# Optimization experiments

Measured on AMD Instinct MI355X. Metric: run time of the kernel, lower is better.

The kernel has to match this reference:

```python
import jax, jax.numpy as jnp
import numpy as np

# dims: S temporal frames, B batch, N queries/batch, K knn neighbors, M img samples, C channels
S, B, N, K, M, C = 3, 2, 2048, 16, 32, 256
W_SCALE = 0.02


def setup_inputs() -> dict:
    key = jax.random.key(0)
    ks = jax.random.split(key, 24)
    f = lambda k, shp: jax.random.normal(k, shp, dtype=jnp.float32)
    w = lambda k, shp: f(k, shp) * W_SCALE
    mask = jax.random.uniform(ks[5], (B, N, M)) > 0.3
    mask = mask.at[..., 0].set(True)  # every query attends to >=1 sample (mirrors `valid` filter)
    return {
        "pts_query_feats": f(ks[0], (B, N, C)),
        "pts_query_pe": f(ks[1], (B, N, C)),
        "knn_feat": f(ks[2], (S, B, N, K, C)),
        "knn_pe": f(ks[3], (S, B, N, K, C)),
        "sampled_feat": f(ks[4], (B, N, M, C)),
        # per-seq temporal MHA (1 head) weights, stacked over S
        "Wq_t": w(ks[6], (S, C, C)), "Wk_t": w(ks[7], (S, C, C)),
        "Wv_t": w(ks[8], (S, C, C)), "Wo_t": w(ks[9], (S, C, C)),
        "bq_t": jnp.zeros((S, C)), "bk_t": jnp.zeros((S, C)),
        "bv_t": jnp.zeros((S, C)), "bo_t": jnp.zeros((S, C)),
        # cross-sensor MHA (1 head) weights
        "Wq_c": w(ks[10], (C, C)), "Wk_c": w(ks[11], (C, C)),
        "Wv_c": w(ks[12], (C, C)), "Wo_c": w(ks[13], (C, C)),
        "bq_c": jnp.zeros((C,)), "bk_c": jnp.zeros((C,)),
        "bv_c": jnp.zeros((C,)), "bo_c": jnp.zeros((C,)),
        "mask": mask,
    }


def reference(pts_query_feats, pts_query_pe, knn_feat, knn_pe, sampled_feat,
              Wq_t, Wk_t, Wv_t, Wo_t, bq_t, bk_t, bv_t, bo_t,
              Wq_c, Wk_c, Wv_c, Wo_c, bq_c, bk_c, bv_c, bo_c, mask):
    C_ = pts_query_feats.shape[-1]
    scale = 1.0 / np.float32(np.sqrt(C_))

    # query = pts features + positional embedding (with_pos_embed)
    q0 = pts_query_feats + pts_query_pe                     # [B,N,C]
    kv = knn_feat + knn_pe                                  # [S,B,N,K,C]

    # per-seq temporal attention (seq_len cloned 1-head MHA), summed over seq
    q = jnp.einsum('bnc,scd->sbnd', q0, Wq_t) + bq_t[:, None, None, :]
    k = jnp.einsum('sbnkc,scd->sbnkd', kv, Wk_t) + bk_t[:, None, None, None, :]
    v = jnp.einsum('sbnkc,scd->sbnkd', kv, Wv_t) + bv_t[:, None, None, None, :]
    attn = jax.nn.softmax(jnp.einsum('sbnd,sbnkd->sbnk', q, k) * scale, axis=-1)
    av = jnp.einsum('sbnk,sbnkd->sbnd', attn, v)
    out = (jnp.einsum('sbnd,sde->sbne', av, Wo_t) + bo_t[:, None, None, :]).sum(0)  # [B,N,C]

    # cross-sensor attention: query = temporal output, key/value = sampled image feats,
    # boolean mask (True = valid; original passes attn_mask = ~mask)
    q2 = out @ Wq_c + bq_c                                  # [B,N,C]
    k2 = jnp.einsum('bnmc,cd->bnmd', sampled_feat, Wk_c) + bk_c
    v2 = jnp.einsum('bnmc,cd->bnmd', sampled_feat, Wv_c) + bv_c
    s2 = jnp.einsum('bnd,bnmd->bnm', q2, k2) * scale
    s2 = jnp.where(mask, s2, jnp.float32(-1e30))
    a2 = jax.nn.softmax(s2, axis=-1)
    cs = jnp.einsum('bnm,bnmd->bnd', a2, v2) @ Wo_c + bo_c  # [B,N,C]
    return cs
```

## Files before the change

### kernel.cpp

```cpp
#include <hip/hip_runtime.h>
#include <hip/hip_bf16.h>
#include <math.h>

#define SS 3
#define BB 2
#define NN 2048
#define KK 16
#define MM 32
#define CC 256
#define BN_TOT 4096
#define SCALE 0.0625f

#define OFF_ACAT   0
#define OFF_ABCAT  196608
#define OFF_VOCAT  197376
#define OFF_VBSUM  393984
#define OFF_AC     394240
#define OFF_ABC    459776
#define OFF_VOC    460032
#define OFF_VBC    525568
#define OFF_A2     525824
#define OFF_AB2    722432
#define OFF_QKCAT  722688
#define OFF_WKV    3868416
#define OFF_QK2    7014144
#define OFF_WS2    8062720

__device__ __forceinline__ void combine_body(const float* __restrict__ L,
                                             const float* __restrict__ R,
                                             float* __restrict__ O, int ldo,
                                             int nt, int r0) {
    __shared__ float L8[8][256];
    int t = threadIdx.x;
#pragma unroll
    for (int j = 0; j < 8; ++j) L8[j][t] = L[(r0 + j) * 256 + t];
    __syncthreads();
    float acc[8] = {};
    if (nt) {
        const float* rp = R + t * 256;
        for (int d = 0; d < 256; d += 4) {
            float4 rv = *(const float4*)(rp + d);
#pragma unroll
            for (int j = 0; j < 8; ++j) {
                float4 lv = *(const float4*)(&L8[j][d]);
                acc[j] += lv.x * rv.x + lv.y * rv.y + lv.z * rv.z + lv.w * rv.w;
            }
        }
    } else {
        for (int d = 0; d < 256; d += 4) {
            float r0v = R[(d + 0) * 256 + t];
            float r1v = R[(d + 1) * 256 + t];
            float r2v = R[(d + 2) * 256 + t];
            float r3v = R[(d + 3) * 256 + t];
#pragma unroll
            for (int j = 0; j < 8; ++j) {
                float4 lv = *(const float4*)(&L8[j][d]);
                acc[j] += lv.x * r0v + lv.y * r1v + lv.z * r2v + lv.w * r3v;
            }
        }
    }
#pragma unroll
    for (int j = 0; j < 8; ++j) O[(r0 + j) * ldo + t] = acc[j];
}

__global__ __launch_bounds__(256) void combine1(
    const float* __restrict__ Wq_t, const float* __restrict__ Wk_t,
    const float* __restrict__ Wv_t, const float* __restrict__ Wo_t,
    const float* __restrict__ Wq_c, const float* __restrict__ Wk_c,
    const float* __restrict__ Wv_c, const float* __restrict__ Wo_c,
    float* __restrict__ ws) {
    int job = blockIdx.x >> 5, rb = blockIdx.x & 31;
    const float *L, *R; float* O; int ldo, nt;
    if (job < 3)       { L = Wq_t + job * 65536; R = Wk_t + job * 65536; O = ws + OFF_ACAT + job * 256;    ldo = 768; nt = 1; }
    else if (job < 6)  { int s = job - 3; L = Wv_t + s * 65536; R = Wo_t + s * 65536; O = ws + OFF_VOCAT + s * 65536; ldo = 256; nt = 0; }
    else if (job == 6) { L = Wq_c; R = Wk_c; O = ws + OFF_AC;  ldo = 256; nt = 1; }
    else               { L = Wv_c; R = Wo_c; O = ws + OFF_VOC; ldo = 256; nt = 0; }
    combine_body(L, R, O, ldo, nt, rb * 8);
}

__global__ __launch_bounds__(256) void bias1(
    const float* __restrict__ Wk_t, const float* __restrict__ Wo_t,
    const float* __restrict__ bq_t, const float* __restrict__ bv_t, const float* __restrict__ bo_t,
    const float* __restrict__ Wk_c, const float* __restrict__ Wo_c,
    const float* __restrict__ bq_c, const float* __restrict__ bv_c, const float* __restrict__ bo_c,
    float* __restrict__ ws) {
    int t = threadIdx.x;
    for (int s = 0; s < 3; ++s) {
        const float* wk = Wk_t + (s * 256 + t) * 256;
        const float* bq = bq_t + s * 256;
        float a = 0;
        for (int d = 0; d < 256; ++d) a += bq[d] * wk[d];
        ws[OFF_ABCAT + s * 256 + t] = a;
    }
    float v = 0;
    for (int s = 0; s < 3; ++s) {
        const float* wo = Wo_t + s * 65536;
        const float* bv = bv_t + s * 256;
        float a = 0;
        for (int d = 0; d < 256; ++d) a += bv[d] * wo[d * 256 + t];
        v += a + bo_t[s * 256 + t];
    }
    ws[OFF_VBSUM + t] = v;
    { float a = 0; const float* wk = Wk_c + t * 256;
      for (int d = 0; d < 256; ++d) a += bq_c[d] * wk[d];
      ws[OFF_ABC + t] = a; }
    { float a = 0;
      for (int d = 0; d < 256; ++d) a += bv_c[d] * Wo_c[d * 256 + t];
      ws[OFF_VBC + t] = a + bo_c[t]; }
}

__global__ __launch_bounds__(256) void combine2(float* __restrict__ ws) {
    int wg = blockIdx.x;
    if (wg < 96) {
        combine_body(ws + OFF_VOCAT, ws + OFF_AC, ws + OFF_A2, 256, 0, wg * 8);
    } else {
        int t = threadIdx.x;
        float a = 0;
        const float* vb = ws + OFF_VBSUM;
        const float* Ac = ws + OFF_AC;
        for (int e = 0; e < 256; ++e) a += vb[e] * Ac[e * 256 + t];
        ws[OFF_AB2 + t] = a + ws[OFF_ABC + t];
    }
}

__global__ __launch_bounds__(256) void gemm_bias(
    const float* __restrict__ A, const float* __restrict__ Aadd, int lda,
    const float* __restrict__ Bm, int ldb,
    const float* __restrict__ bias,
    float* __restrict__ out, int ldo, int Kd) {
    __shared__ float As[16][64];
    __shared__ float Bs[16][68];
    int tid = threadIdx.x;
    int bm = blockIdx.x * 64, bn = blockIdx.y * 64;
    int tx = tid & 15, ty = tid >> 4;
    float acc[4][4] = {};
    int ar = tid >> 2, ak = (tid & 3) * 4;
    int bk = tid >> 4, bq = (tid & 15) * 4;
    const float* Ab  = A + (size_t)(bm + ar) * lda + ak;
    const float* A2b = Aadd ? Aadd + (size_t)(bm + ar) * lda + ak : nullptr;
    const float* Bb  = Bm + (size_t)bk * ldb + bn + bq;
    for (int k0 = 0; k0 < Kd; k0 += 16) {
        float4 av = *(const float4*)(Ab + k0);
        if (Aadd) {
            float4 a2 = *(const float4*)(A2b + k0);
            av.x += a2.x; av.y += a2.y; av.z += a2.z; av.w += a2.w;
        }
        As[ak + 0][ar] = av.x; As[ak + 1][ar] = av.y;
        As[ak + 2][ar] = av.z; As[ak + 3][ar] = av.w;
        *(float4*)(&Bs[bk][bq]) = *(const float4*)(Bb + (size_t)k0 * ldb);
        __syncthreads();
#pragma unroll
        for (int kk = 0; kk < 16; ++kk) {
            float4 a4 = *(const float4*)(&As[kk][ty * 4]);
            float4 b4 = *(const float4*)(&Bs[kk][tx * 4]);
            float aa[4] = {a4.x, a4.y, a4.z, a4.w};
            float bb[4] = {b4.x, b4.y, b4.z, b4.w};
#pragma unroll
            for (int i = 0; i < 4; ++i)
#pragma unroll
                for (int j = 0; j < 4; ++j) acc[i][j] += aa[i] * bb[j];
        }
        __syncthreads();
    }
#pragma unroll
    for (int i = 0; i < 4; ++i) {
        int row = bm + ty * 4 + i;
        float b0 = bias[bn + tx * 4 + 0], b1 = bias[bn + tx * 4 + 1];
        float b2 = bias[bn + tx * 4 + 2], b3 = bias[bn + tx * 4 + 3];
        float4 o;
        o.x = acc[i][0] + b0; o.y = acc[i][1] + b1;
        o.z = acc[i][2] + b2; o.w = acc[i][3] + b3;
        *(float4*)(&out[(size_t)row * ldo + bn + tx * 4]) = o;
    }
}

__global__ __launch_bounds__(256) void attn_temporal(
    const float* __restrict__ knn_feat, const float* __restrict__ knn_pe,
    const float* __restrict__ qk_cat, float* __restrict__ wkv_cat) {
    int wg = blockIdx.x;
    int s = wg >> 12, bn = wg & 4095;
    int t = threadIdx.x;
    int lane = t & 63, wv = t >> 6;
    size_t base = (size_t)wg * 4096 + t;
    float kv[16];
#pragma unroll
    for (int k = 0; k < 16; ++k)
        kv[k] = knn_feat[base + k * 256] + knn_pe[base + k * 256];
    float qv = qk_cat[(size_t)bn * 768 + s * 256 + t];
    __shared__ float red[4][16];
    __shared__ float sc[16];
#pragma unroll
    for (int k = 0; k < 16; ++k) {
        float v = qv * kv[k];
#pragma unroll
        for (int off = 32; off; off >>= 1) v += __shfl_xor(v, off, 64);
        if (lane == 0) red[wv][k] = v;
    }
    __syncthreads();
    if (t < 16) sc[t] = (red[0][t] + red[1][t] + red[2][t] + red[3][t]) * SCALE;
    __syncthreads();
    float mx = -1e30f;
#pragma unroll
    for (int k = 0; k < 16; ++k) mx = fmaxf(mx, sc[k]);
    float p[16], den = 0.f;
#pragma unroll
    for (int k = 0; k < 16; ++k) { p[k] = __expf(sc[k] - mx); den += p[k]; }
    float o = 0.f;
#pragma unroll
    for (int k = 0; k < 16; ++k) o += p[k] * kv[k];
    wkv_cat[(size_t)bn * 768 + s * 256 + t] = o * (1.f / den);
}

__global__ __launch_bounds__(256) void attn_cross(
    const float* __restrict__ sampled, const int* __restrict__ mask,
    const float* __restrict__ qk2, float* __restrict__ ws2) {
    int bn = blockIdx.x;
    int t = threadIdx.x;
    int lane = t & 63, wv = t >> 6;
    size_t base = (size_t)bn * 8192 + t;
    float smp[32];
#pragma unroll
    for (int m = 0; m < 32; ++m) smp[m] = sampled[base + m * 256];
    float qv = qk2[(size_t)bn * 256 + t];
    __shared__ float red[4][32];
    __shared__ float sc[32];
#pragma unroll
    for (int m = 0; m < 32; ++m) {
        float v = qv * smp[m];
#pragma unroll
        for (int off = 32; off; off >>= 1) v += __shfl_xor(v, off, 64);
        if (lane == 0) red[wv][m] = v;
    }
    __syncthreads();
    if (t < 32) {
        float v = (red[0][t] + red[1][t] + red[2][t] + red[3][t]) * SCALE;
        sc[t] = mask[(size_t)bn * 32 + t] ? v : -1e30f;
    }
    __syncthreads();
    float mx = -1e30f;
#pragma unroll
    for (int m = 0; m < 32; ++m) mx = fmaxf(mx, sc[m]);
    float den = 0.f, o = 0.f;
#pragma unroll
    for (int m = 0; m < 32; ++m) {
        float p = __expf(sc[m] - mx);
        den += p; o += p * smp[m];
    }
    ws2[(size_t)bn * 256 + t] = o / den;
}

extern "C" void kernel_launch(void* const* d_in, const int* in_sizes, int n_in,
                              void* d_out, int out_size, void* d_ws, size_t ws_size,
                              hipStream_t stream) {
    const float* feats    = (const float*)d_in[0];
    const float* pe       = (const float*)d_in[1];
    const float* knn_feat = (const float*)d_in[2];
    const float* knn_pe   = (const float*)d_in[3];
    const float* sampled  = (const float*)d_in[4];
    const float* Wq_t = (const float*)d_in[5];
    const float* Wk_t = (const float*)d_in[6];
    const float* Wv_t = (const float*)d_in[7];
    const float* Wo_t = (const float*)d_in[8];
    const float* bq_t = (const float*)d_in[9];
    const float* bv_t = (const float*)d_in[11];
    const float* bo_t = (const float*)d_in[12];
    const float* Wq_c = (const float*)d_in[13];
    const float* Wk_c = (const float*)d_in[14];
    const float* Wv_c = (const float*)d_in[15];
    const float* Wo_c = (const float*)d_in[16];
    const float* bq_c = (const float*)d_in[17];
    const float* bv_c = (const float*)d_in[19];
    const float* bo_c = (const float*)d_in[20];
    const int*   mask = (const int*)d_in[21];
    float* ws  = (float*)d_ws;
    float* out = (float*)d_out;

    hipLaunchKernelGGL(combine1, dim3(256), dim3(256), 0, stream,
                       Wq_t, Wk_t, Wv_t, Wo_t, Wq_c, Wk_c, Wv_c, Wo_c, ws);
    hipLaunchKernelGGL(bias1, dim3(1), dim3(256), 0, stream,
                       Wk_t, Wo_t, bq_t, bv_t, bo_t, Wk_c, Wo_c, bq_c, bv_c, bo_c, ws);
    hipLaunchKernelGGL(combine2, dim3(97), dim3(256), 0, stream, ws);
    hipLaunchKernelGGL(gemm_bias, dim3(64, 12), dim3(256), 0, stream,
                       feats, pe, 256, ws + OFF_ACAT, 768, ws + OFF_ABCAT,
                       ws + OFF_QKCAT, 768, 256);
    hipLaunchKernelGGL(attn_temporal, dim3(12288), dim3(256), 0, stream,
                       knn_feat, knn_pe, ws + OFF_QKCAT, ws + OFF_WKV);
    hipLaunchKernelGGL(gemm_bias, dim3(64, 4), dim3(256), 0, stream,
                       ws + OFF_WKV, nullptr, 768, ws + OFF_A2, 256, ws + OFF_AB2,
                       ws + OFF_QK2, 256, 768);
    hipLaunchKernelGGL(attn_cross, dim3(4096), dim3(256), 0, stream,
                       sampled, mask, ws + OFF_QK2, ws + OFF_WS2);
    hipLaunchKernelGGL(gemm_bias, dim3(64, 4), dim3(256), 0, stream,
                       ws + OFF_WS2, nullptr, 256, ws + OFF_VOC, 256, ws + OFF_VBC,
                       out, 256, 256);
}
```

Baseline: 730.1 us.

## Wave-per-unit attention kernels, fold bias kernel into combine, drop GEMM B staging

The temporal attention kernel now gives each 64-lane wavefront one (s,b,n) unit, using float4 loads and a transpose-style shuffle reduction. This removes the LDS reductions and __syncthreads barriers that the old one-block-per-unit layout needed. The cross attention kernel splits the 32 samples across 4 waves with float4 loads and combines partial outputs through LDS. The single-block bias kernel is merged into combine1 as 5 extra blocks, saving a launch and its serial tail. gemm_bias now reads B directly from global memory instead of staging it in LDS, which may raise global traffic in exchange for fewer LDS stores.

```diff
diff --git a/kernel.cpp b/kernel.cpp
--- a/kernel.cpp
+++ b/kernel.cpp
@@ -68,7 +68,40 @@
     const float* __restrict__ Wv_t, const float* __restrict__ Wo_t,
     const float* __restrict__ Wq_c, const float* __restrict__ Wk_c,
     const float* __restrict__ Wv_c, const float* __restrict__ Wo_c,
+    const float* __restrict__ bq_t, const float* __restrict__ bv_t,
+    const float* __restrict__ bo_t,
+    const float* __restrict__ bq_c, const float* __restrict__ bv_c,
+    const float* __restrict__ bo_c,
     float* __restrict__ ws) {
+    int t = threadIdx.x;
+    if (blockIdx.x >= 256) {
+        int jb = blockIdx.x - 256;
+        if (jb < 3) {
+            const float* wk = Wk_t + (jb * 256 + t) * 256;
+            const float* bq = bq_t + jb * 256;
+            float a = 0;
+            for (int d = 0; d < 256; ++d) a += bq[d] * wk[d];
+            ws[OFF_ABCAT + jb * 256 + t] = a;
+        } else if (jb == 3) {
+            float v = 0;
+            for (int s = 0; s < 3; ++s) {
+                const float* wo = Wo_t + s * 65536;
+                const float* bv = bv_t + s * 256;
+                float a = 0;
+                for (int d = 0; d < 256; ++d) a += bv[d] * wo[d * 256 + t];
+                v += a + bo_t[s * 256 + t];
+            }
+            ws[OFF_VBSUM + t] = v;
+        } else {
+            float a = 0; const float* wk = Wk_c + t * 256;
+            for (int d = 0; d < 256; ++d) a += bq_c[d] * wk[d];
+            ws[OFF_ABC + t] = a;
+            float b = 0;
+            for (int d = 0; d < 256; ++d) b += bv_c[d] * Wo_c[d * 256 + t];
+            ws[OFF_VBC + t] = b + bo_c[t];
+        }
+        return;
+    }
     int job = blockIdx.x >> 5, rb = blockIdx.x & 31;
     const float *L, *R; float* O; int ldo, nt;
     if (job < 3)       { L = Wq_t + job * 65536; R = Wk_t + job * 65536; O = ws + OFF_ACAT + job * 256;    ldo = 768; nt = 1; }
@@ -76,37 +109,6 @@
     else if (job == 6) { L = Wq_c; R = Wk_c; O = ws + OFF_AC;  ldo = 256; nt = 1; }
     else               { L = Wv_c; R = Wo_c; O = ws + OFF_VOC; ldo = 256; nt = 0; }
     combine_body(L, R, O, ldo, nt, rb * 8);
-}
-
-__global__ __launch_bounds__(256) void bias1(
-    const float* __restrict__ Wk_t, const float* __restrict__ Wo_t,
-    const float* __restrict__ bq_t, const float* __restrict__ bv_t, const float* __restrict__ bo_t,
-    const float* __restrict__ Wk_c, const float* __restrict__ Wo_c,
-    const float* __restrict__ bq_c, const float* __restrict__ bv_c, const float* __restrict__ bo_c,
-    float* __restrict__ ws) {
-    int t = threadIdx.x;
-    for (int s = 0; s < 3; ++s) {
-        const float* wk = Wk_t + (s * 256 + t) * 256;
-        const float* bq = bq_t + s * 256;
-        float a = 0;
-        for (int d = 0; d < 256; ++d) a += bq[d] * wk[d];
-        ws[OFF_ABCAT + s * 256 + t] = a;
-    }
-    float v = 0;
-    for (int s = 0; s < 3; ++s) {
-        const float* wo = Wo_t + s * 65536;
-        const float* bv = bv_t + s * 256;
-        float a = 0;
-        for (int d = 0; d < 256; ++d) a += bv[d] * wo[d * 256 + t];
-        v += a + bo_t[s * 256 + t];
-    }
-    ws[OFF_VBSUM + t] = v;
-    { float a = 0; const float* wk = Wk_c + t * 256;
-      for (int d = 0; d < 256; ++d) a += bq_c[d] * wk[d];
-      ws[OFF_ABC + t] = a; }
-    { float a = 0;
-      for (int d = 0; d < 256; ++d) a += bv_c[d] * Wo_c[d * 256 + t];
-      ws[OFF_VBC + t] = a + bo_c[t]; }
 }
 
 __global__ __launch_bounds__(256) void combine2(float* __restrict__ ws) {
@@ -128,17 +130,15 @@
     const float* __restrict__ Bm, int ldb,
     const float* __restrict__ bias,
     float* __restrict__ out, int ldo, int Kd) {
-    __shared__ float As[16][64];
-    __shared__ float Bs[16][68];
+    __shared__ float As[16][68];
     int tid = threadIdx.x;
     int bm = blockIdx.x * 64, bn = blockIdx.y * 64;
     int tx = tid & 15, ty = tid >> 4;
     float acc[4][4] = {};
     int ar = tid >> 2, ak = (tid & 3) * 4;
-    int bk = tid >> 4, bq = (tid & 15) * 4;
     const float* Ab  = A + (size_t)(bm + ar) * lda + ak;
     const float* A2b = Aadd ? Aadd + (size_t)(bm + ar) * lda + ak : nullptr;
-    const float* Bb  = Bm + (size_t)bk * ldb + bn + bq;
+    const float* Bb  = Bm + bn + tx * 4;
     for (int k0 = 0; k0 < Kd; k0 += 16) {
         float4 av = *(const float4*)(Ab + k0);
         if (Aadd) {
@@ -147,12 +147,11 @@
         }
         As[ak + 0][ar] = av.x; As[ak + 1][ar] = av.y;
         As[ak + 2][ar] = av.z; As[ak + 3][ar] = av.w;
-        *(float4*)(&Bs[bk][bq]) = *(const float4*)(Bb + (size_t)k0 * ldb);
         __syncthreads();
 #pragma unroll
         for (int kk = 0; kk < 16; ++kk) {
+            float4 b4 = *(const float4*)(Bb + (size_t)(k0 + kk) * ldb);
             float4 a4 = *(const float4*)(&As[kk][ty * 4]);
-            float4 b4 = *(const float4*)(&Bs[kk][tx * 4]);
             float aa[4] = {a4.x, a4.y, a4.z, a4.w};
             float bb[4] = {b4.x, b4.y, b4.z, b4.w};
 #pragma unroll
@@ -177,38 +176,68 @@
 __global__ __launch_bounds__(256) void attn_temporal(
     const float* __restrict__ knn_feat, const float* __restrict__ knn_pe,
     const float* __restrict__ qk_cat, float* __restrict__ wkv_cat) {
-    int wg = blockIdx.x;
-    int s = wg >> 12, bn = wg & 4095;
-    int t = threadIdx.x;
-    int lane = t & 63, wv = t >> 6;
-    size_t base = (size_t)wg * 4096 + t;
-    float kv[16];
+    int unit = blockIdx.x * 4 + (threadIdx.x >> 6);
+    int lane = threadIdx.x & 63;
+    int s = unit >> 12, bn = unit & 4095;
+    size_t base = (size_t)unit * 4096 + lane * 4;
+    float4 kv[16];
+#pragma unroll
+    for (int k = 0; k < 16; ++k) {
+        float4 f = *(const float4*)(knn_feat + base + k * 256);
+        float4 p = *(const float4*)(knn_pe   + base + k * 256);
+        kv[k] = make_float4(f.x + p.x, f.y + p.y, f.z + p.z, f.w + p.w);
+    }
+    float4 q = *(const float4*)(qk_cat + (size_t)bn * 768 + s * 256 + lane * 4);
+    float v[16];
 #pragma unroll
     for (int k = 0; k < 16; ++k)
-        kv[k] = knn_feat[base + k * 256] + knn_pe[base + k * 256];
-    float qv = qk_cat[(size_t)bn * 768 + s * 256 + t];
-    __shared__ float red[4][16];
-    __shared__ float sc[16];
+        v[k] = q.x * kv[k].x + q.y * kv[k].y + q.z * kv[k].z + q.w * kv[k].w;
+    { int hi = lane & 32;
+#pragma unroll
+      for (int j = 0; j < 8; ++j) {
+          float send = hi ? v[j] : v[j + 8];
+          float keep = hi ? v[j + 8] : v[j];
+          v[j] = keep + __shfl_xor(send, 32, 64);
+      } }
+    { int hi = lane & 16;
+#pragma unroll
+      for (int j = 0; j < 4; ++j) {
+          float send = hi ? v[j] : v[j + 4];
+          float keep = hi ? v[j + 4] : v[j];
+          v[j] = keep + __shfl_xor(send, 16, 64);
+      } }
+    { int hi = lane & 8;
+#pragma unroll
+      for (int j = 0; j < 2; ++j) {
+          float send = hi ? v[j] : v[j + 2];
+          float keep = hi ? v[j + 2] : v[j];
+          v[j] = keep + __shfl_xor(send, 8, 64);
+      } }
+    { int hi = lane & 4;
+      float send = hi ? v[0] : v[1];
+      float keep = hi ? v[1] : v[0];
+      v[0] = keep + __shfl_xor(send, 4, 64); }
+    float r = v[0];
+    r += __shfl_xor(r, 1, 64);
+    r += __shfl_xor(r, 2, 64);
+    float sc[16];
+#pragma unroll
+    for (int k = 0; k < 16; ++k) sc[k] = __shfl(r, k << 2, 64) * SCALE;
+    float mx = sc[0];
+#pragma unroll
+    for (int k = 1; k < 16; ++k) mx = fmaxf(mx, sc[k]);
+    float den = 0.f;
+#pragma unroll
+    for (int k = 0; k < 16; ++k) { sc[k] = __expf(sc[k] - mx); den += sc[k]; }
+    float inv = 1.f / den;
+    float ox = 0, oy = 0, oz = 0, ow = 0;
 #pragma unroll
     for (int k = 0; k < 16; ++k) {
-        float v = qv * kv[k];
-#pragma unroll
-        for (int off = 32; off; off >>= 1) v += __shfl_xor(v, off, 64);
-        if (lane == 0) red[wv][k] = v;
-    }
-    __syncthreads();
-    if (t < 16) sc[t] = (red[0][t] + red[1][t] + red[2][t] + red[3][t]) * SCALE;
-    __syncthreads();
-    float mx = -1e30f;
-#pragma unroll
-    for (int k = 0; k < 16; ++k) mx = fmaxf(mx, sc[k]);
-    float p[16], den = 0.f;
-#pragma unroll
-    for (int k = 0; k < 16; ++k) { p[k] = __expf(sc[k] - mx); den += p[k]; }
-    float o = 0.f;
-#pragma unroll
-    for (int k = 0; k < 16; ++k) o += p[k] * kv[k];
-    wkv_cat[(size_t)bn * 768 + s * 256 + t] = o * (1.f / den);
+        ox += sc[k] * kv[k].x; oy += sc[k] * kv[k].y;
+        oz += sc[k] * kv[k].z; ow += sc[k] * kv[k].w;
+    }
+    float4 o = make_float4(ox * inv, oy * inv, oz * inv, ow * inv);
+    *(float4*)(wkv_cat + (size_t)bn * 768 + s * 256 + lane * 4) = o;
 }
 
 __global__ __launch_bounds__(256) void attn_cross(
@@ -216,37 +245,76 @@
     const float* __restrict__ qk2, float* __restrict__ ws2) {
     int bn = blockIdx.x;
     int t = threadIdx.x;
-    int lane = t & 63, wv = t >> 6;
-    size_t base = (size_t)bn * 8192 + t;
-    float smp[32];
-#pragma unroll
-    for (int m = 0; m < 32; ++m) smp[m] = sampled[base + m * 256];
-    float qv = qk2[(size_t)bn * 256 + t];
-    __shared__ float red[4][32];
-    __shared__ float sc[32];
+    int w = t >> 6, lane = t & 63;
+    __shared__ float sc_lds[32];
+    __shared__ float obuf[4][256];
+    size_t base = (size_t)bn * 8192 + (size_t)(w * 8) * 256 + lane * 4;
+    float4 sm[8];
+#pragma unroll
+    for (int j = 0; j < 8; ++j) sm[j] = *(const float4*)(sampled + base + j * 256);
+    float4 q = *(const float4*)(qk2 + (size_t)bn * 256 + lane * 4);
+    float v[8];
+#pragma unroll
+    for (int j = 0; j < 8; ++j)
+        v[j] = q.x * sm[j].x + q.y * sm[j].y + q.z * sm[j].z + q.w * sm[j].w;
+    { int hi = lane & 32;
+#pragma unroll
+      for (int j = 0; j < 4; ++j) {
+          float send = hi ? v[j] : v[j + 4];
+          float keep = hi ? v[j + 4] : v[j];
+          v[j] = keep + __shfl_xor(send, 32, 64);
+      } }
+    { int hi = lane & 16;
+#pragma unroll
+      for (int j = 0; j < 2; ++j) {
+          float send = hi ? v[j] : v[j + 2];
+          float keep = hi ? v[j + 2] : v[j];
+          v[j] = keep + __shfl_xor(send, 16, 64);
+      } }
+    { int hi = lane & 8;
+      float send = hi ? v[0] : v[1];
+      float keep = hi ? v[1] : v[0];
+      v[0] = keep + __shfl_xor(send, 8, 64); }
+    float r = v[0];
+    r += __shfl_xor(r, 1, 64);
+    r += __shfl_xor(r, 2, 64);
+    r += __shfl_xor(r, 4, 64);
+    if ((lane & 7) == 0) {
+        int m = w * 8 + (lane >> 3);
+        int valid = mask[(size_t)bn * 32 + m];
+        sc_lds[m] = valid ? r * SCALE : -1e30f;
+    }
+    __syncthreads();
+    float scv[32];
+#pragma unroll
+    for (int i = 0; i < 8; ++i) {
+        float4 v4 = *(const float4*)(&sc_lds[i * 4]);
+        scv[i * 4 + 0] = v4.x; scv[i * 4 + 1] = v4.y;
+        scv[i * 4 + 2] = v4.z; scv[i * 4 + 3] = v4.w;
+    }
+    float mx = scv[0];
+#pragma unroll
+    for (int m = 1; m < 32; ++m) mx = fmaxf(mx, scv[m]);
+    float den = 0.f;
+    float el[8] = {};
 #pragma unroll
     for (int m = 0; m < 32; ++m) {
-        float v = qv * smp[m];
-#pragma unroll
-        for (int off = 32; off; off >>= 1) v += __shfl_xor(v, off, 64);
-        if (lane == 0) red[wv][m] = v;
-    }
+        float ex = __expf(scv[m] - mx);
+        den += ex;
+        el[m & 7] = ((m >> 3) == w) ? ex : el[m & 7];
+    }
+    float inv = 1.f / den;
+    float ox = 0, oy = 0, oz = 0, ow = 0;
+#pragma unroll
+    for (int j = 0; j < 8; ++j) {
+        ox += el[j] * sm[j].x; oy += el[j] * sm[j].y;
+        oz += el[j] * sm[j].z; ow += el[j] * sm[j].w;
+    }
+    *(float4*)(&obuf[w][lane * 4]) =
+        make_float4(ox * inv, oy * inv, oz * inv, ow * inv);
     __syncthreads();
-    if (t < 32) {
-        float v = (red[0][t] + red[1][t] + red[2][t] + red[3][t]) * SCALE;
-        sc[t] = mask[(size_t)bn * 32 + t] ? v : -1e30f;
-    }
-    __syncthreads();
-    float mx = -1e30f;
-#pragma unroll
-    for (int m = 0; m < 32; ++m) mx = fmaxf(mx, sc[m]);
-    float den = 0.f, o = 0.f;
-#pragma unroll
-    for (int m = 0; m < 32; ++m) {
-        float p = __expf(sc[m] - mx);
-        den += p; o += p * smp[m];
-    }
-    ws2[(size_t)bn * 256 + t] = o / den;
+    float o = obuf[0][t] + obuf[1][t] + obuf[2][t] + obuf[3][t];
+    ws2[(size_t)bn * 256 + t] = o;
 }
 
 extern "C" void kernel_launch(void* const* d_in, const int* in_sizes, int n_in,
@@ -275,15 +343,14 @@
     float* ws  = (float*)d_ws;
     float* out = (float*)d_out;
 
-    hipLaunchKernelGGL(combine1, dim3(256), dim3(256), 0, stream,
-                       Wq_t, Wk_t, Wv_t, Wo_t, Wq_c, Wk_c, Wv_c, Wo_c, ws);
-    hipLaunchKernelGGL(bias1, dim3(1), dim3(256), 0, stream,
-                       Wk_t, Wo_t, bq_t, bv_t, bo_t, Wk_c, Wo_c, bq_c, bv_c, bo_c, ws);
+    hipLaunchKernelGGL(combine1, dim3(261), dim3(256), 0, stream,
+                       Wq_t, Wk_t, Wv_t, Wo_t, Wq_c, Wk_c, Wv_c, Wo_c,
+                       bq_t, bv_t, bo_t, bq_c, bv_c, bo_c, ws);
     hipLaunchKernelGGL(combine2, dim3(97), dim3(256), 0, stream, ws);
     hipLaunchKernelGGL(gemm_bias, dim3(64, 12), dim3(256), 0, stream,
                        feats, pe, 256, ws + OFF_ACAT, 768, ws + OFF_ABCAT,
                        ws + OFF_QKCAT, 768, 256);
-    hipLaunchKernelGGL(attn_temporal, dim3(12288), dim3(256), 0, stream,
+    hipLaunchKernelGGL(attn_temporal, dim3(3072), dim3(256), 0, stream,
                        knn_feat, knn_pe, ws + OFF_QKCAT, ws + OFF_WKV);
     hipLaunchKernelGGL(gemm_bias, dim3(64, 4), dim3(256), 0, stream,
                        ws + OFF_WKV, nullptr, 768, ws + OFF_A2, 256, ws + OFF_AB2,
```

After: 702.7 us. -3.8%, faster.
